# Kernel optimization log

Hardware: AMD Instinct MI355X
Metric: run time of the kernel (lower is better)

## Reference

```python
import jax, jax.numpy as jnp
import numpy as np

# Device / mapping constants from the source (is_low_resistance=True branch)
V_REF = 0.25
G_MIN = 0.1
G_MAX = 1.0
K_V = 2.0 * V_REF  # x_to_V scale
N_AVG = 2.18
N_STD = 0.115


def setup_inputs() -> dict:
    key = jax.random.key(0)
    k_x, k_wp, k_wn, k_n = jax.random.split(key, 4)
    n_in, n_out, batch = 1024, 512, 128
    stdv = 1.0 / np.sqrt(n_in)
    x = jax.random.uniform(k_x, (batch, n_in), dtype=jnp.float32)
    w_pos = 0.5 + stdv * jax.random.normal(k_wp, (n_in, n_out), dtype=jnp.float32)
    w_neg = 0.5 + stdv * jax.random.normal(k_wn, (n_in, n_out), dtype=jnp.float32)
    b_pos = 0.5 * jnp.ones((n_out,), jnp.float32)
    b_neg = 0.5 * jnp.ones((n_out,), jnp.float32)
    # per-device I-V nonlinearity parameter n ~ N(n_avg, n_std), one per crossbar cell
    n_param = N_AVG + N_STD * jax.random.normal(k_n, (n_in + 1, 2 * n_out), dtype=jnp.float32)
    return {"x": x, "w_pos": w_pos, "w_neg": w_neg, "b_pos": b_pos, "b_neg": b_neg,
            "n_param": n_param}


def _memristor_dense(x, w_pos, w_neg, b_pos, b_neg, n_param):
    x = jnp.clip(x, 0.0, 1.0)
    # append bias rows, interleave pos/neg along output axis -> (n_in+1, 2*n_out)
    cw_pos = jnp.concatenate([w_pos, b_pos[None, :]], axis=0)
    cw_neg = jnp.concatenate([w_neg, b_neg[None, :]], axis=0)
    w = jnp.stack([cw_pos, cw_neg], axis=-1).reshape(cw_pos.shape[0], -1)
    # append ones column to inputs (bias voltage line)
    inp = jnp.concatenate([x, jnp.ones((x.shape[0], 1), x.dtype)], axis=1)  # (B, n_in+1)
    # weight -> effective conductance (differential scheme), then offset by G_min
    max_w = jnp.max(jnp.abs(w))
    k_G = (G_MAX - G_MIN) / max_w
    G = jnp.abs(k_G * w) + G_MIN  # (n_in+1, 2*n_out)
    # input -> voltage
    V = K_V * inp  # (B, n_in+1)
    # nonlinear-parameter I-V model: I = sign(V) * G * V_ref * (|V|/V_ref) ** (log2(n) + 1)
    # (satisfies n = I(2*V_ref) / (2 * I(V_ref)))
    exponent = jnp.log2(n_param) + 1.0  # (n_in+1, 2*n_out)
    v_ratio = jnp.abs(V) / V_REF  # (B, n_in+1)
    vr = v_ratio[:, :, None]  # (B, n_in+1, 1)
    vr_safe = jnp.where(vr > 0, vr, 1.0)
    pow_term = jnp.where(vr > 0, vr_safe ** exponent[None, :, :], 0.0)  # (B, n_in+1, 2*n_out)
    I_ind = jnp.sign(V)[:, :, None] * (G * V_REF)[None, :, :] * pow_term
    # sum currents along bit lines
    I = jnp.sum(I_ind, axis=1)  # (B, 2*n_out)
    # currents -> outputs (differential pairs are interleaved)
    y = (I[:, 0::2] - I[:, 1::2]) / (K_V * k_G)  # (B, n_out)
    return y


def reference(x, w_pos, w_neg, b_pos, b_neg, n_param):
    return _memristor_dense(x, w_pos, w_neg, b_pos, b_neg, n_param)
```

## Files before the change

kernel.cpp:

```cpp
#include <hip/hip_runtime.h>
#include <hip/hip_bf16.h>


#define LOG2F(v)  __builtin_amdgcn_logf(v)
#define EXP2F(v)  __builtin_amdgcn_exp2f(v)

#define NJ 16
#define NB 64
#define KI 32
#define SLS4 17

__global__ __launch_bounds__(256) void setup_kernel(
    const float* __restrict__ w_pos, const float* __restrict__ w_neg,
    const float* __restrict__ b_pos, const float* __restrict__ b_neg,
    float* __restrict__ y, int* __restrict__ ws) {
  const int t = threadIdx.x, blk = blockIdx.x;
  float4* y4 = (float4*)y;
  if (t < 64) y4[blk * 64 + t] = make_float4(0.f, 0.f, 0.f, 0.f);
  const float4* wp4 = (const float4*)w_pos;
  const float4* wn4 = (const float4*)w_neg;
  float m = 0.0f;
  #pragma unroll
  for (int r = 0; r < 2; ++r) {
    int i = blk * 512 + r * 256 + t;
    float4 a = wp4[i], b = wn4[i];
    m = fmaxf(m, fmaxf(fmaxf(fabsf(a.x), fabsf(a.y)), fmaxf(fabsf(a.z), fabsf(a.w))));
    m = fmaxf(m, fmaxf(fmaxf(fabsf(b.x), fabsf(b.y)), fmaxf(fabsf(b.z), fabsf(b.w))));
  }
  if (blk == 0) {
    m = fmaxf(m, fmaxf(fabsf(b_pos[t]), fabsf(b_pos[t + 256])));
    m = fmaxf(m, fmaxf(fabsf(b_neg[t]), fabsf(b_neg[t + 256])));
  }
  #pragma unroll
  for (int off = 32; off > 0; off >>= 1)
    m = fmaxf(m, __shfl_down(m, off, 64));
  __shared__ float sm[4];
  int lane = t & 63, wv = t >> 6;
  if (lane == 0) sm[wv] = m;
  __syncthreads();
  if (t == 0) {
    m = fmaxf(fmaxf(sm[0], sm[1]), fmaxf(sm[2], sm[3]));
    atomicMax(ws, __float_as_int(m));
  }
}

__global__ __launch_bounds__(256) void memristor_kernel(
    const float* __restrict__ x, const float* __restrict__ w_pos,
    const float* __restrict__ w_neg, const float* __restrict__ b_pos,
    const float* __restrict__ b_neg, const float* __restrict__ n_param,
    const float* __restrict__ ws, float* __restrict__ y) {
  __shared__ float2 sPa[KI * NJ];
  __shared__ float2 sPb[KI * NJ];
  __shared__ float4 sL4[KI * SLS4];

  const float mw = __int_as_float(((const int*)ws)[0]);
  const float c0 = mw * (0.05f / 0.9f);

  const int j0 = blockIdx.x * NJ;
  const int b0 = blockIdx.y * NB;
  const int zt = blockIdx.z;
  const int i0 = zt * KI;
  const int t  = threadIdx.x;
  const int jj = t & 15;
  const int bq = t >> 4;

  const float2* np2 = (const float2*)n_param;

  #pragma unroll
  for (int r = 0; r < 2; ++r) {
    int il = r * 16 + (t >> 4);
    int jl = t & 15;
    int gi = i0 + il;
    float wp = w_pos[gi * 512 + j0 + jl];
    float wn = w_neg[gi * 512 + j0 + jl];
    float2 np = np2[gi * 512 + j0 + jl];
    sPa[il * NJ + jl] = make_float2(fmaf(0.5f, fabsf(wp), c0), LOG2F(np.x) + 1.0f);
    sPb[il * NJ + jl] = make_float2(fmaf(0.5f, fabsf(wn), c0), LOG2F(np.y) + 1.0f);
  }
  {
    float* sL = (float*)sL4;
    const float4* x4 = (const float4*)x;
    #pragma unroll
    for (int r = 0; r < 2; ++r) {
      int row = r * 32 + (t >> 3);
      int k4  = t & 7;
      float4 v = x4[(b0 + row) * 256 + zt * 8 + k4];
      v.x = fminf(fmaxf(v.x, 0.0f), 1.0f);
      v.y = fminf(fmaxf(v.y, 0.0f), 1.0f);
      v.z = fminf(fmaxf(v.z, 0.0f), 1.0f);
      v.w = fminf(fmaxf(v.w, 0.0f), 1.0f);
      sL[(4 * k4 + 0) * (4 * SLS4) + row] = LOG2F(2.0f * v.x);
      sL[(4 * k4 + 1) * (4 * SLS4) + row] = LOG2F(2.0f * v.y);
      sL[(4 * k4 + 2) * (4 * SLS4) + row] = LOG2F(2.0f * v.z);
      sL[(4 * k4 + 3) * (4 * SLS4) + row] = LOG2F(2.0f * v.w);
    }
  }
  __syncthreads();

  float a0 = 0.0f, a1 = 0.0f, a2 = 0.0f, a3 = 0.0f;
  #pragma unroll 4
  for (int k = 0; k < KI; ++k) {
    float2 pa = sPa[k * NJ + jj];
    float2 pb = sPb[k * NJ + jj];
    float4 l  = sL4[k * SLS4 + bq];
    a0 = fmaf(pa.x, EXP2F(pa.y * l.x), fmaf(-pb.x, EXP2F(pb.y * l.x), a0));
    a1 = fmaf(pa.x, EXP2F(pa.y * l.y), fmaf(-pb.x, EXP2F(pb.y * l.y), a1));
    a2 = fmaf(pa.x, EXP2F(pa.y * l.z), fmaf(-pb.x, EXP2F(pb.y * l.z), a2));
    a3 = fmaf(pa.x, EXP2F(pa.y * l.w), fmaf(-pb.x, EXP2F(pb.y * l.w), a3));
  }

  if (zt == 31) {
    int jg = j0 + jj;
    float2 np = np2[1024 * 512 + jg];
    float p0 = fmaf(0.5f, fabsf(b_pos[jg]), c0);
    float p1 = fmaf(0.5f, fabsf(b_neg[jg]), c0);
    float bias = p0 * EXP2F(LOG2F(np.x) + 1.0f) - p1 * EXP2F(LOG2F(np.y) + 1.0f);
    a0 += bias; a1 += bias; a2 += bias; a3 += bias;
  }

  const int row0 = b0 + 4 * bq;
  atomicAdd(&y[(row0 + 0) * 512 + j0 + jj], a0);
  atomicAdd(&y[(row0 + 1) * 512 + j0 + jj], a1);
  atomicAdd(&y[(row0 + 2) * 512 + j0 + jj], a2);
  atomicAdd(&y[(row0 + 3) * 512 + j0 + jj], a3);
}

extern "C" void kernel_launch(void* const* d_in, const int* in_sizes, int n_in,
                              void* d_out, int out_size, void* d_ws, size_t ws_size,
                              hipStream_t stream) {
  const float* x       = (const float*)d_in[0];
  const float* w_pos   = (const float*)d_in[1];
  const float* w_neg   = (const float*)d_in[2];
  const float* b_pos   = (const float*)d_in[3];
  const float* b_neg   = (const float*)d_in[4];
  const float* n_param = (const float*)d_in[5];
  float* y   = (float*)d_out;

  setup_kernel<<<dim3(256), dim3(256), 0, stream>>>(
      w_pos, w_neg, b_pos, b_neg, y, (int*)d_ws);

  memristor_kernel<<<dim3(32, 2, 32), dim3(256), 0, stream>>>(
      x, w_pos, w_neg, b_pos, b_neg, n_param, (const float*)d_ws, y);
}
```

Measured before the change: 87.46 us.

## Replace split-K atomic accumulation with partial buffers and a separate reduce kernel

Each split-K block now writes its partial sums to a workspace buffer instead of doing atomicAdd into the output. A third kernel sums the 32 partials per output element, and the output zeroing is dropped from the setup kernel. The aim is to remove contention and the latency of float atomics on the output. The cost is an extra kernel launch and about 8 MB of partial-sum traffic written and then read back.

```diff
diff --git a/kernel.cpp b/kernel.cpp
--- a/kernel.cpp
+++ b/kernel.cpp
@@ -9,14 +9,13 @@
 #define NB 64
 #define KI 32
 #define SLS4 17
+#define PART_OFF 1024
 
 __global__ __launch_bounds__(256) void setup_kernel(
     const float* __restrict__ w_pos, const float* __restrict__ w_neg,
     const float* __restrict__ b_pos, const float* __restrict__ b_neg,
-    float* __restrict__ y, int* __restrict__ ws) {
+    int* __restrict__ ws) {
   const int t = threadIdx.x, blk = blockIdx.x;
-  float4* y4 = (float4*)y;
-  if (t < 64) y4[blk * 64 + t] = make_float4(0.f, 0.f, 0.f, 0.f);
   const float4* wp4 = (const float4*)w_pos;
   const float4* wn4 = (const float4*)w_neg;
   float m = 0.0f;
@@ -48,7 +47,7 @@
     const float* __restrict__ x, const float* __restrict__ w_pos,
     const float* __restrict__ w_neg, const float* __restrict__ b_pos,
     const float* __restrict__ b_neg, const float* __restrict__ n_param,
-    const float* __restrict__ ws, float* __restrict__ y) {
+    float* __restrict__ ws) {
   __shared__ float2 sPa[KI * NJ];
   __shared__ float2 sPb[KI * NJ];
   __shared__ float4 sL4[KI * SLS4];
@@ -118,11 +117,33 @@
     a0 += bias; a1 += bias; a2 += bias; a3 += bias;
   }
 
-  const int row0 = b0 + 4 * bq;
-  atomicAdd(&y[(row0 + 0) * 512 + j0 + jj], a0);
-  atomicAdd(&y[(row0 + 1) * 512 + j0 + jj], a1);
-  atomicAdd(&y[(row0 + 2) * 512 + j0 + jj], a2);
-  atomicAdd(&y[(row0 + 3) * 512 + j0 + jj], a3);
+  float* part = ((float*)ws) + PART_OFF;
+  const int s = blockIdx.y * 32 + zt;
+  float* p = part + (s * 64 + 4 * bq) * 512 + j0 + jj;
+  p[0 * 512] = a0;
+  p[1 * 512] = a1;
+  p[2 * 512] = a2;
+  p[3 * 512] = a3;
+}
+
+__global__ __launch_bounds__(256) void reduce_kernel(
+    const float* __restrict__ ws, float* __restrict__ y) {
+  const float* part = ws + PART_OFF;
+  const int g = blockIdx.x * 256 + threadIdx.x;
+  const int b = g >> 9;
+  const int j = g & 511;
+  const int by = b >> 6;
+  const int r  = b & 63;
+  const float* p = part + (by * 2048 + r) * 512 + j;
+  float s0 = 0.0f, s1 = 0.0f, s2 = 0.0f, s3 = 0.0f;
+  #pragma unroll
+  for (int z = 0; z < 32; z += 4) {
+    s0 += p[(z + 0) * 32768];
+    s1 += p[(z + 1) * 32768];
+    s2 += p[(z + 2) * 32768];
+    s3 += p[(z + 3) * 32768];
+  }
+  y[g] = (s0 + s1) + (s2 + s3);
 }
 
 extern "C" void kernel_launch(void* const* d_in, const int* in_sizes, int n_in,
@@ -137,8 +158,11 @@
   float* y   = (float*)d_out;
 
   setup_kernel<<<dim3(256), dim3(256), 0, stream>>>(
-      w_pos, w_neg, b_pos, b_neg, y, (int*)d_ws);
+      w_pos, w_neg, b_pos, b_neg, (int*)d_ws);
 
   memristor_kernel<<<dim3(32, 2, 32), dim3(256), 0, stream>>>(
-      x, w_pos, w_neg, b_pos, b_neg, n_param, (const float*)d_ws, y);
+      x, w_pos, w_neg, b_pos, b_neg, n_param, (float*)d_ws);
+
+  reduce_kernel<<<dim3(256), dim3(256), 0, stream>>>(
+      (const float*)d_ws, y);
 }
```

New measurement: 92.46 us. 5.7% more time.
